# Kernel optimization log

Measured on AMD Instinct MI355X. Metric: run time of the kernel, lower is better.

Reference implementation:

```python
import jax, jax.numpy as jnp
import numpy as np

IGNORE_INDEX = -100
N, H, V = 4096, 4096, 32000


def setup_inputs() -> dict:
    key = jax.random.key(0)
    k1, k2, k3 = jax.random.split(key, 3)
    x = jax.random.normal(k1, (N, H), dtype=jnp.float32)
    y = jax.random.randint(k2, (N,), 0, V, dtype=jnp.int64)
    # lm_head weight, torch Linear layout [out_features=V, in_features=H]
    W = jax.random.normal(k3, (V, H), dtype=jnp.float32) * (1.0 / np.sqrt(H))
    return {"x": x, "y": y, "W": W}


def reference(x, y, W):
    # Fused linear + cross-entropy, reduction='mean' over non-ignored tokens.
    logits = jnp.einsum("nh,vh->nv", x, W)            # [N, V]
    logp = jax.nn.log_softmax(logits, axis=-1)         # [N, V]
    safe_y = jnp.where(y == IGNORE_INDEX, 0, y)
    nll = -jnp.take_along_axis(logp, safe_y[:, None], axis=-1)[:, 0]  # [N]
    valid = (y != IGNORE_INDEX).astype(logits.dtype)
    n_valid = jnp.maximum(valid.sum(), 1.0)
    return (nll * valid).sum() / n_valid
```

## Files before the change

kernel.cpp:

```cpp
#include <hip/hip_runtime.h>
#include <stdint.h>
#include <math.h>

#define N_TOK 4096
#define H_DIM 4096
#define V_DIM 32000

#define BM2 256
#define BN2 256
#define BK2 64
#define NKT (H_DIM / BK2)
#define CT2 (V_DIM / BN2)
#define MT2 (N_TOK / BM2)
#define WSCALE 16.0f
#define WSCALE_INV 0.0625f

#define BM 128
#define BN 128
#define BK 64
#define CT_NUM (V_DIM / BN)
#define MT_NUM (N_TOK / BM)

typedef __attribute__((ext_vector_type(8))) short short8;
typedef __attribute__((ext_vector_type(4))) float f32x4;
typedef __attribute__((ext_vector_type(2))) long long2_t;

#define MFMA16(a, b, c) __builtin_amdgcn_mfma_f32_16x16x32_bf16(a, b, c, 0, 0, 0)
#define MFMAF8(a, b, c) __builtin_amdgcn_mfma_f32_16x16x32_fp8_fp8(a, b, c, 0, 0, 0)
#define BARRIER() asm volatile("s_barrier" ::: "memory")

__device__ __forceinline__ unsigned short f2bf(float x) {
  union { float f; unsigned int u; } v; v.f = x;
  unsigned int r = v.u + 0x7fffu + ((v.u >> 16) & 1u);
  return (unsigned short)(r >> 16);
}

__device__ __forceinline__ unsigned int pk4(float a, float b, float c, float d) {
  int v = __builtin_amdgcn_cvt_pk_fp8_f32(a, b, 0, false);
  v = __builtin_amdgcn_cvt_pk_fp8_f32(c, d, v, true);
  return (unsigned int)v;
}

__device__ __forceinline__ void async16(const void* g, void* lds) {
  __builtin_amdgcn_global_load_lds(
      (const __attribute__((address_space(1))) void*)g,
      (__attribute__((address_space(3))) void*)lds, 16, 0, 0);
}

__global__ __launch_bounds__(256) void cast_f32_to_fp8_perm(
    const float* __restrict__ in, uint4* __restrict__ out, long nslots,
    float scale) {
  long stride = (long)gridDim.x * blockDim.x;
  for (long slot = (long)blockIdx.x * blockDim.x + threadIdx.x; slot < nslots;
       slot += stride) {
    long b = slot >> 2;
    int s = (int)(slot & 3);
    const float* p0 = in + b * 64 + s * 8;
    const float* p1 = p0 + 32;
    float4 a0 = *(const float4*)p0, a1 = *(const float4*)(p0 + 4);
    float4 c0 = *(const float4*)p1, c1 = *(const float4*)(p1 + 4);
    uint4 o;
    o.x = pk4(a0.x * scale, a0.y * scale, a0.z * scale, a0.w * scale);
    o.y = pk4(a1.x * scale, a1.y * scale, a1.z * scale, a1.w * scale);
    o.z = pk4(c0.x * scale, c0.y * scale, c0.z * scale, c0.w * scale);
    o.w = pk4(c1.x * scale, c1.y * scale, c1.z * scale, c1.w * scale);
    out[slot] = o;
  }
}

__device__ __forceinline__ void stage8(const uint8_t* __restrict__ src,
                                       int grow0, int kt, char* dest, int tid) {
  const int r = tid >> 2;
  const int p = tid & 3;
  const int s = p ^ (r & 3);
  const uint8_t* g = src + (size_t)(grow0 + r) * H_DIM + (size_t)kt * 64 + s * 16;
  async16(g, dest + (tid >> 6) * 1024);
}

template<int MF>
__device__ __forceinline__ void cluster16f8(f32x4 (&acc)[8][4],
    long2_t aL, long2_t aH, long2_t (&breg)[4]) {
#pragma unroll
  for (int nf = 0; nf < 4; nf++) acc[MF][nf]     = MFMAF8(aL[0], breg[nf][0], acc[MF][nf]);
#pragma unroll
  for (int nf = 0; nf < 4; nf++) acc[MF + 1][nf] = MFMAF8(aH[0], breg[nf][0], acc[MF + 1][nf]);
#pragma unroll
  for (int nf = 0; nf < 4; nf++) acc[MF][nf]     = MFMAF8(aL[1], breg[nf][1], acc[MF][nf]);
#pragma unroll
  for (int nf = 0; nf < 4; nf++) acc[MF + 1][nf] = MFMAF8(aH[1], breg[nf][1], acc[MF + 1][nf]);
}

template<int P>
__device__ __forceinline__ void phase_tile(char* lds,
    const uint8_t* __restrict__ Xq, const uint8_t* __restrict__ Wq,
    int mbase, int cbase, int ktA, int ktB, int tid,
    const int (&aOff)[8], const int (&bOff)[4], f32x4 (&acc)[8][4]) {
  const char* aB = lds + P * 32768;
  const char* bB = aB + 16384;
  char* aN = lds + (P ^ 1) * 32768;
  char* bC = lds + P * 32768 + 16384;
  long2_t breg[4];

  stage8(Xq, mbase + 0, ktA, aN + 0, tid);
#pragma unroll
  for (int nf = 0; nf < 4; nf++) breg[nf] = *(const long2_t*)(bB + bOff[nf]);
  {
    long2_t a0 = *(const long2_t*)(aB + aOff[0]);
    long2_t a1 = *(const long2_t*)(aB + aOff[1]);
    BARRIER();
    __builtin_amdgcn_s_setprio(1);
    cluster16f8<0>(acc, a0, a1, breg);
    __builtin_amdgcn_s_setprio(0);
    BARRIER();
  }
  stage8(Xq, mbase + 128, ktA, aN + 8192, tid);
  {
    long2_t a0 = *(const long2_t*)(aB + aOff[2]);
    long2_t a1 = *(const long2_t*)(aB + aOff[3]);
    BARRIER();
    __builtin_amdgcn_s_setprio(1);
    cluster16f8<2>(acc, a0, a1, breg);
    __builtin_amdgcn_s_setprio(0);
    BARRIER();
  }
  stage8(Wq, cbase + 0, ktB, bC + 0, tid);
  {
    long2_t a0 = *(const long2_t*)(aB + aOff[4]);
    long2_t a1 = *(const long2_t*)(aB + aOff[5]);
    BARRIER();
    __builtin_amdgcn_s_setprio(1);
    cluster16f8<4>(acc, a0, a1, breg);
    __builtin_amdgcn_s_setprio(0);
    BARRIER();
  }
  stage8(Wq, cbase + 128, ktB, bC + 8192, tid);
  {
    long2_t a0 = *(const long2_t*)(aB + aOff[6]);
    long2_t a1 = *(const long2_t*)(aB + aOff[7]);
    asm volatile("s_waitcnt vmcnt(2)" ::: "memory");
    BARRIER();
    __builtin_amdgcn_s_setprio(1);
    cluster16f8<6>(acc, a0, a1, breg);
    __builtin_amdgcn_s_setprio(0);
    BARRIER();
  }
}

__global__ __launch_bounds__(512, 2) void gemm_lse8(
    const uint8_t* __restrict__ Xq, const uint8_t* __restrict__ Wq,
    float* __restrict__ pmax, float* __restrict__ psum) {
  extern __shared__ char lds[];
  const int tid = threadIdx.x;
  const int lane = tid & 63;
  const int wid = tid >> 6;
  const int wm = wid >> 2, wn = wid & 3;

  int logical = (blockIdx.x & 7) * (CT2 * MT2 / 8) + (blockIdx.x >> 3);
  const int ct = logical / MT2, mt = logical - ct * MT2;
  const int mbase = mt * BM2, cbase = ct * BN2;

  const int sl16 = (((lane >> 4) ^ (lane & 3)) << 4);
  int aOff[8], bOff[4];
#pragma unroll
  for (int mf = 0; mf < 8; mf++)
    aOff[mf] = (wm * 128 + mf * 16 + (lane & 15)) * 64 + sl16;
#pragma unroll
  for (int nf = 0; nf < 4; nf++)
    bOff[nf] = (wn * 64 + nf * 16 + (lane & 15)) * 64 + sl16;

  f32x4 acc[8][4];
#pragma unroll
  for (int i = 0; i < 8; i++)
#pragma unroll
    for (int j = 0; j < 4; j++) { f32x4 z = {0.f, 0.f, 0.f, 0.f}; acc[i][j] = z; }

  stage8(Wq, cbase + 0,   0, lds + 16384, tid);
  stage8(Wq, cbase + 128, 0, lds + 24576, tid);
  stage8(Xq, mbase + 0,   0, lds + 0,     tid);
  stage8(Xq, mbase + 128, 0, lds + 8192,  tid);
  stage8(Wq, cbase + 0,   1, lds + 49152, tid);
  stage8(Wq, cbase + 128, 1, lds + 57344, tid);
  asm volatile("s_waitcnt vmcnt(2)" ::: "memory");
  BARRIER();

#pragma unroll 1
  for (int i = 0; i < NKT / 2; i++) {
    int g0 = 2 * i, g1 = 2 * i + 1;
    int a0t = g0 + 1;
    int b0t = (g0 + 2 < NKT) ? g0 + 2 : NKT - 1;
    int a1t = (g1 + 1 < NKT) ? g1 + 1 : NKT - 1;
    int b1t = (g1 + 2 < NKT) ? g1 + 2 : NKT - 1;
    phase_tile<0>(lds, Xq, Wq, mbase, cbase, a0t, b0t, tid, aOff, bOff, acc);
    phase_tile<1>(lds, Xq, Wq, mbase, cbase, a1t, b1t, tid, aOff, bOff, acc);
  }

  asm volatile("s_waitcnt vmcnt(0)" ::: "memory");
  __syncthreads();

  float2* red = (float2*)lds;
#pragma unroll
  for (int mf = 0; mf < 8; mf++) {
#pragma unroll
    for (int qq = 0; qq < 4; qq++) {
      float v0 = acc[mf][0][qq] * WSCALE_INV, v1 = acc[mf][1][qq] * WSCALE_INV;
      float v2 = acc[mf][2][qq] * WSCALE_INV, v3 = acc[mf][3][qq] * WSCALE_INV;
      float mx = fmaxf(fmaxf(v0, v1), fmaxf(v2, v3));
#pragma unroll
      for (int d = 1; d < 16; d <<= 1) mx = fmaxf(mx, __shfl_xor(mx, d));
      float se = __expf(v0 - mx) + __expf(v1 - mx) + __expf(v2 - mx) + __expf(v3 - mx);
#pragma unroll
      for (int d = 1; d < 16; d <<= 1) se += __shfl_xor(se, d);
      if ((lane & 15) == 0) {
        int row = (wm << 7) + mf * 16 + ((lane >> 4) << 2) + qq;
        float2 v; v.x = mx; v.y = se;
        red[row * 4 + wn] = v;
      }
    }
  }
  __syncthreads();
  if (tid < 256) {
    float M = -INFINITY, S = 0.f;
#pragma unroll
    for (int w = 0; w < 4; w++) {
      float2 rr = red[tid * 4 + w];
      float Mn = fmaxf(M, rr.x);
      S = S * __expf(M - Mn) + rr.y * __expf(rr.x - Mn);
      M = Mn;
    }
    size_t o = (size_t)ct * N_TOK + mbase + tid;
    pmax[o] = M;
    psum[o] = S;
  }
}

__global__ __launch_bounds__(256) void gemm_lse_small(
    const float* __restrict__ Xf, const float* __restrict__ Wf,
    float* __restrict__ pmax, float* __restrict__ psum) {
  __shared__ unsigned short As[BM * BK];
  __shared__ unsigned short Bs[BN * BK];
  const int ct = blockIdx.x / MT_NUM;
  const int mt = blockIdx.x % MT_NUM;
  const int mbase = mt * BM, cbase = ct * BN;
  const int tid = threadIdx.x;
  const int lane = tid & 63;
  const int wid = tid >> 6;
  const int wr = wid >> 1, wc = wid & 1;
  f32x4 acc[4][4];
#pragma unroll
  for (int i = 0; i < 4; i++)
#pragma unroll
    for (int j = 0; j < 4; j++) { f32x4 z = {0.f, 0.f, 0.f, 0.f}; acc[i][j] = z; }
  for (int ks = 0; ks < H_DIM / BK; ks++) {
    const int k0 = ks * BK;
#pragma unroll
    for (int r = 0; r < 4; r++) {
      int o = r * 4096 + wid * 1024 + lane * 16;
      int row = o >> 7;
      int kc = (o & 127) >> 1;
      const float* xs = Xf + (size_t)(mbase + row) * H_DIM + k0 + kc;
      const float* wv = Wf + (size_t)(cbase + row) * H_DIM + k0 + kc;
      float4 x0 = *(const float4*)xs, x1 = *(const float4*)(xs + 4);
      float4 w0 = *(const float4*)wv, w1 = *(const float4*)(wv + 4);
      short8 xa, wa;
      xa[0] = f2bf(x0.x); xa[1] = f2bf(x0.y); xa[2] = f2bf(x0.z); xa[3] = f2bf(x0.w);
      xa[4] = f2bf(x1.x); xa[5] = f2bf(x1.y); xa[6] = f2bf(x1.z); xa[7] = f2bf(x1.w);
      wa[0] = f2bf(w0.x); wa[1] = f2bf(w0.y); wa[2] = f2bf(w0.z); wa[3] = f2bf(w0.w);
      wa[4] = f2bf(w1.x); wa[5] = f2bf(w1.y); wa[6] = f2bf(w1.z); wa[7] = f2bf(w1.w);
      *(short8*)((char*)As + o) = xa;
      *(short8*)((char*)Bs + o) = wa;
    }
    __syncthreads();
#pragma unroll
    for (int kk = 0; kk < 2; kk++) {
      short8 a[4], b[4];
#pragma unroll
      for (int m = 0; m < 4; m++)
        a[m] = *(const short8*)((const char*)As +
                (wr * 64 + m * 16 + (lane & 15)) * 128 + kk * 64 + (lane >> 4) * 16);
#pragma unroll
      for (int n = 0; n < 4; n++)
        b[n] = *(const short8*)((const char*)Bs +
                (wc * 64 + n * 16 + (lane & 15)) * 128 + kk * 64 + (lane >> 4) * 16);
#pragma unroll
      for (int m = 0; m < 4; m++)
#pragma unroll
        for (int n = 0; n < 4; n++)
          acc[m][n] = MFMA16(a[m], b[n], acc[m][n]);
    }
    __syncthreads();
  }
  float* red = (float*)As;
  const int g = lane >> 4;
#pragma unroll
  for (int m = 0; m < 4; m++) {
#pragma unroll
    for (int q = 0; q < 4; q++) {
      float v0 = acc[m][0][q], v1 = acc[m][1][q], v2 = acc[m][2][q], v3 = acc[m][3][q];
      float mx = fmaxf(fmaxf(v0, v1), fmaxf(v2, v3));
#pragma unroll
      for (int d = 1; d < 16; d <<= 1) mx = fmaxf(mx, __shfl_xor(mx, d));
      float se = __expf(v0 - mx) + __expf(v1 - mx) + __expf(v2 - mx) + __expf(v3 - mx);
#pragma unroll
      for (int d = 1; d < 16; d <<= 1) se += __shfl_xor(se, d);
      if ((lane & 15) == 0) {
        int row = wr * 64 + m * 16 + g * 4 + q;
        red[row * 4 + wc * 2 + 0] = mx;
        red[row * 4 + wc * 2 + 1] = se;
      }
    }
  }
  __syncthreads();
  if (tid < BM) {
    float m0 = red[tid * 4 + 0], s0 = red[tid * 4 + 1];
    float m1 = red[tid * 4 + 2], s1 = red[tid * 4 + 3];
    float M = fmaxf(m0, m1);
    float S = s0 * __expf(m0 - M) + s1 * __expf(m1 - M);
    size_t o = (size_t)ct * N_TOK + mbase + tid;
    pmax[o] = M;
    psum[o] = S;
  }
}

__global__ __launch_bounds__(256) void target_logit(
    const float* __restrict__ X, const float* __restrict__ W,
    const int* __restrict__ y, float* __restrict__ tl) {
  __shared__ float red[4];
  int row = blockIdx.x;
  int lab = y[row];
  float s = 0.f;
  if (lab >= 0 && lab < V_DIM) {
    const float4* xr = (const float4*)(X + (size_t)row * H_DIM);
    const float4* wr = (const float4*)(W + (size_t)lab * H_DIM);
    for (int i = threadIdx.x; i < H_DIM / 4; i += 256) {
      float4 a = xr[i], b = wr[i];
      s += a.x * b.x + a.y * b.y + a.z * b.z + a.w * b.w;
    }
  }
#pragma unroll
  for (int o = 32; o > 0; o >>= 1) s += __shfl_down(s, o);
  if ((threadIdx.x & 63) == 0) red[threadIdx.x >> 6] = s;
  __syncthreads();
  if (threadIdx.x == 0) tl[row] = red[0] + red[1] + red[2] + red[3];
}

__global__ __launch_bounds__(256) void combine_rows(
    const float* __restrict__ pmax, const float* __restrict__ psum,
    const float* __restrict__ tl, const int* __restrict__ y,
    float* __restrict__ lossb, float* __restrict__ validb, int n_ct) {
  int row = blockIdx.x * 256 + threadIdx.x;
  if (row >= N_TOK) return;
  float M = -INFINITY, S = 0.f;
  for (int ct = 0; ct < n_ct; ct++) {
    float m = pmax[(size_t)ct * N_TOK + row];
    float s = psum[(size_t)ct * N_TOK + row];
    float Mn = fmaxf(M, m);
    S = S * __expf(M - Mn) + s * __expf(m - Mn);
    M = Mn;
  }
  bool valid = (y[row] != -100);
  lossb[row] = valid ? (M + __logf(S) - tl[row]) : 0.f;
  validb[row] = valid ? 1.f : 0.f;
}

__global__ __launch_bounds__(256) void finalize_loss(
    const float* __restrict__ lossb, const float* __restrict__ validb,
    float* __restrict__ out) {
  __shared__ float rs[4], rc[4];
  float s = 0.f, c = 0.f;
  for (int i = threadIdx.x; i < N_TOK; i += 256) { s += lossb[i]; c += validb[i]; }
#pragma unroll
  for (int o = 32; o > 0; o >>= 1) { s += __shfl_down(s, o); c += __shfl_down(c, o); }
  if ((threadIdx.x & 63) == 0) { rs[threadIdx.x >> 6] = s; rc[threadIdx.x >> 6] = c; }
  __syncthreads();
  if (threadIdx.x == 0) {
    float S = rs[0] + rs[1] + rs[2] + rs[3];
    float C = rc[0] + rc[1] + rc[2] + rc[3];
    out[0] = S / fmaxf(C, 1.f);
  }
}

extern "C" void kernel_launch(void* const* d_in, const int* in_sizes, int n_in,
                              void* d_out, int out_size, void* d_ws, size_t ws_size,
                              hipStream_t stream) {
  const float* x = (const float*)d_in[0];
  const int* y = (const int*)d_in[1];
  const float* W = (const float*)d_in[2];
  float* out = (float*)d_out;
  char* ws = (char*)d_ws;

  const size_t szWq = (size_t)V_DIM * H_DIM;
  const size_t szXq = (size_t)N_TOK * H_DIM;
  const size_t szP  = (size_t)CT_NUM * N_TOK * 4;
  const size_t szT  = (size_t)N_TOK * 4;
  const size_t needFull = szWq + szXq + 2 * szP + 3 * szT;

  bool full = (ws_size >= needFull);
  uint8_t* Wq = nullptr;
  uint8_t* Xq = nullptr;
  size_t off = 0;
  if (full) { Wq = (uint8_t*)ws; Xq = (uint8_t*)(ws + szWq); off = szWq + szXq; }
  float* pmax   = (float*)(ws + off); off += szP;
  float* psum   = (float*)(ws + off); off += szP;
  float* tl     = (float*)(ws + off); off += szT;
  float* lossb  = (float*)(ws + off); off += szT;
  float* validb = (float*)(ws + off);

  if (full) {
    cast_f32_to_fp8_perm<<<8192, 256, 0, stream>>>(
        W, (uint4*)Wq, (long)(szWq / 16), WSCALE);
    cast_f32_to_fp8_perm<<<2048, 256, 0, stream>>>(
        x, (uint4*)Xq, (long)(szXq / 16), 1.0f);
    (void)hipFuncSetAttribute((const void*)gemm_lse8,
        hipFuncAttributeMaxDynamicSharedMemorySize, 65536);
    gemm_lse8<<<CT2 * MT2, 512, 65536, stream>>>(Xq, Wq, pmax, psum);
    target_logit<<<N_TOK, 256, 0, stream>>>(x, W, y, tl);
    combine_rows<<<N_TOK / 256, 256, 0, stream>>>(pmax, psum, tl, y, lossb, validb, CT2);
  } else {
    gemm_lse_small<<<CT_NUM * MT_NUM, 256, 0, stream>>>(x, W, pmax, psum);
    target_logit<<<N_TOK, 256, 0, stream>>>(x, W, y, tl);
    combine_rows<<<N_TOK / 256, 256, 0, stream>>>(pmax, psum, tl, y, lossb, validb, CT_NUM);
  }
  finalize_loss<<<1, 256, 0, stream>>>(lossb, validb, out);
}
```

Baseline: 938.9 us.

## Switch FP8 GEMM to MX-scaled 16x16x128 MFMA with BK=128 tiles

```diff
diff --git a/kernel.cpp b/kernel.cpp
--- a/kernel.cpp
+++ b/kernel.cpp
@@ -8,8 +8,8 @@
 
 #define BM2 256
 #define BN2 256
-#define BK2 64
-#define NKT (H_DIM / BK2)
+#define BK2 128
+#define NKT2 (H_DIM / BK2)
 #define CT2 (V_DIM / BN2)
 #define MT2 (N_TOK / BM2)
 #define WSCALE 16.0f
@@ -23,10 +23,12 @@
 
 typedef __attribute__((ext_vector_type(8))) short short8;
 typedef __attribute__((ext_vector_type(4))) float f32x4;
-typedef __attribute__((ext_vector_type(2))) long long2_t;
+typedef __attribute__((ext_vector_type(4))) int i32x4;
+typedef __attribute__((ext_vector_type(8))) int i32x8;
 
 #define MFMA16(a, b, c) __builtin_amdgcn_mfma_f32_16x16x32_bf16(a, b, c, 0, 0, 0)
-#define MFMAF8(a, b, c) __builtin_amdgcn_mfma_f32_16x16x32_fp8_fp8(a, b, c, 0, 0, 0)
+#define MFMAMX(a, b, c) __builtin_amdgcn_mfma_scale_f32_16x16x128_f8f6f4( \
+    a, b, c, 0, 0, 0, 0x7f7f7f7f, 0, 0x7f7f7f7f)
 #define BARRIER() asm volatile("s_barrier" ::: "memory")
 
 __device__ __forceinline__ unsigned short f2bf(float x) {
@@ -47,100 +49,109 @@
       (__attribute__((address_space(3))) void*)lds, 16, 0, 0);
 }
 
-__global__ __launch_bounds__(256) void cast_f32_to_fp8_perm(
+__global__ __launch_bounds__(256) void cast_f32_to_fp8(
     const float* __restrict__ in, uint4* __restrict__ out, long nslots,
     float scale) {
   long stride = (long)gridDim.x * blockDim.x;
   for (long slot = (long)blockIdx.x * blockDim.x + threadIdx.x; slot < nslots;
        slot += stride) {
-    long b = slot >> 2;
-    int s = (int)(slot & 3);
-    const float* p0 = in + b * 64 + s * 8;
-    const float* p1 = p0 + 32;
-    float4 a0 = *(const float4*)p0, a1 = *(const float4*)(p0 + 4);
-    float4 c0 = *(const float4*)p1, c1 = *(const float4*)(p1 + 4);
+    const float4* p = (const float4*)(in + slot * 16);
+    float4 a0 = p[0], a1 = p[1], a2 = p[2], a3 = p[3];
     uint4 o;
     o.x = pk4(a0.x * scale, a0.y * scale, a0.z * scale, a0.w * scale);
     o.y = pk4(a1.x * scale, a1.y * scale, a1.z * scale, a1.w * scale);
-    o.z = pk4(c0.x * scale, c0.y * scale, c0.z * scale, c0.w * scale);
-    o.w = pk4(c1.x * scale, c1.y * scale, c1.z * scale, c1.w * scale);
+    o.z = pk4(a2.x * scale, a2.y * scale, a2.z * scale, a2.w * scale);
+    o.w = pk4(a3.x * scale, a3.y * scale, a3.z * scale, a3.w * scale);
     out[slot] = o;
   }
 }
 
-__device__ __forceinline__ void stage8(const uint8_t* __restrict__ src,
-                                       int grow0, int kt, char* dest, int tid) {
-  const int r = tid >> 2;
-  const int p = tid & 3;
-  const int s = p ^ (r & 3);
-  const uint8_t* g = src + (size_t)(grow0 + r) * H_DIM + (size_t)kt * 64 + s * 16;
+__device__ __forceinline__ void stageMX(const uint8_t* __restrict__ src,
+                                        int grow0, int kt, char* dest, int tid) {
+  const int r = tid >> 3;
+  const int p = tid & 7;
+  const int s = p ^ (r & 7);
+  const uint8_t* g = src + (size_t)(grow0 + r) * H_DIM + (size_t)kt * 128 + s * 16;
   async16(g, dest + (tid >> 6) * 1024);
 }
 
-template<int MF>
-__device__ __forceinline__ void cluster16f8(f32x4 (&acc)[8][4],
-    long2_t aL, long2_t aH, long2_t (&breg)[4]) {
-#pragma unroll
-  for (int nf = 0; nf < 4; nf++) acc[MF][nf]     = MFMAF8(aL[0], breg[nf][0], acc[MF][nf]);
-#pragma unroll
-  for (int nf = 0; nf < 4; nf++) acc[MF + 1][nf] = MFMAF8(aH[0], breg[nf][0], acc[MF + 1][nf]);
-#pragma unroll
-  for (int nf = 0; nf < 4; nf++) acc[MF][nf]     = MFMAF8(aL[1], breg[nf][1], acc[MF][nf]);
-#pragma unroll
-  for (int nf = 0; nf < 4; nf++) acc[MF + 1][nf] = MFMAF8(aH[1], breg[nf][1], acc[MF + 1][nf]);
+__device__ __forceinline__ i32x8 ld_op(const char* base, int rowByte, int s0, int s1) {
+  i32x4 lo = *(const i32x4*)(base + rowByte + s0);
+  i32x4 hi = *(const i32x4*)(base + rowByte + s1);
+  i32x8 r;
+  r[0] = lo[0]; r[1] = lo[1]; r[2] = lo[2]; r[3] = lo[3];
+  r[4] = hi[0]; r[5] = hi[1]; r[6] = hi[2]; r[7] = hi[3];
+  return r;
 }
 
 template<int P>
-__device__ __forceinline__ void phase_tile(char* lds,
+__device__ __forceinline__ void tile_mx(char* lds,
     const uint8_t* __restrict__ Xq, const uint8_t* __restrict__ Wq,
     int mbase, int cbase, int ktA, int ktB, int tid,
-    const int (&aOff)[8], const int (&bOff)[4], f32x4 (&acc)[8][4]) {
-  const char* aB = lds + P * 32768;
-  const char* bB = aB + 16384;
-  char* aN = lds + (P ^ 1) * 32768;
-  char* bC = lds + P * 32768 + 16384;
-  long2_t breg[4];
-
-  stage8(Xq, mbase + 0, ktA, aN + 0, tid);
-#pragma unroll
-  for (int nf = 0; nf < 4; nf++) breg[nf] = *(const long2_t*)(bB + bOff[nf]);
+    const int (&aRow)[8], const int (&bRow)[4], int s0, int s1,
+    f32x4 (&acc)[8][4]) {
+  const char* aB = lds + P * 65536;
+  const char* bB = aB + 32768;
+  char* aN = lds + (P ^ 1) * 65536;
+  char* bC = lds + P * 65536 + 32768;
+  i32x8 breg[4];
+
+  stageMX(Xq, mbase + 0,  ktA, aN + 0,    tid);
+  stageMX(Xq, mbase + 64, ktA, aN + 8192, tid);
+#pragma unroll
+  for (int nf = 0; nf < 4; nf++) breg[nf] = ld_op(bB, bRow[nf], s0, s1);
   {
-    long2_t a0 = *(const long2_t*)(aB + aOff[0]);
-    long2_t a1 = *(const long2_t*)(aB + aOff[1]);
+    i32x8 a0 = ld_op(aB, aRow[0], s0, s1);
+    i32x8 a1 = ld_op(aB, aRow[1], s0, s1);
     BARRIER();
     __builtin_amdgcn_s_setprio(1);
-    cluster16f8<0>(acc, a0, a1, breg);
+#pragma unroll
+    for (int nf = 0; nf < 4; nf++) acc[0][nf] = MFMAMX(a0, breg[nf], acc[0][nf]);
+#pragma unroll
+    for (int nf = 0; nf < 4; nf++) acc[1][nf] = MFMAMX(a1, breg[nf], acc[1][nf]);
     __builtin_amdgcn_s_setprio(0);
     BARRIER();
   }
-  stage8(Xq, mbase + 128, ktA, aN + 8192, tid);
+  stageMX(Xq, mbase + 128, ktA, aN + 16384, tid);
+  stageMX(Xq, mbase + 192, ktA, aN + 24576, tid);
   {
-    long2_t a0 = *(const long2_t*)(aB + aOff[2]);
-    long2_t a1 = *(const long2_t*)(aB + aOff[3]);
+    i32x8 a0 = ld_op(aB, aRow[2], s0, s1);
+    i32x8 a1 = ld_op(aB, aRow[3], s0, s1);
     BARRIER();
     __builtin_amdgcn_s_setprio(1);
-    cluster16f8<2>(acc, a0, a1, breg);
+#pragma unroll
+    for (int nf = 0; nf < 4; nf++) acc[2][nf] = MFMAMX(a0, breg[nf], acc[2][nf]);
+#pragma unroll
+    for (int nf = 0; nf < 4; nf++) acc[3][nf] = MFMAMX(a1, breg[nf], acc[3][nf]);
     __builtin_amdgcn_s_setprio(0);
     BARRIER();
   }
-  stage8(Wq, cbase + 0, ktB, bC + 0, tid);
+  stageMX(Wq, cbase + 0,  ktB, bC + 0,    tid);
+  stageMX(Wq, cbase + 64, ktB, bC + 8192, tid);
   {
-    long2_t a0 = *(const long2_t*)(aB + aOff[4]);
-    long2_t a1 = *(const long2_t*)(aB + aOff[5]);
+    i32x8 a0 = ld_op(aB, aRow[4], s0, s1);
+    i32x8 a1 = ld_op(aB, aRow[5], s0, s1);
     BARRIER();
     __builtin_amdgcn_s_setprio(1);
-    cluster16f8<4>(acc, a0, a1, breg);
+#pragma unroll
+    for (int nf = 0; nf < 4; nf++) acc[4][nf] = MFMAMX(a0, breg[nf], acc[4][nf]);
+#pragma unroll
+    for (int nf = 0; nf < 4; nf++) acc[5][nf] = MFMAMX(a1, breg[nf], acc[5][nf]);
     __builtin_amdgcn_s_setprio(0);
     BARRIER();
   }
-  stage8(Wq, cbase + 128, ktB, bC + 8192, tid);
+  stageMX(Wq, cbase + 128, ktB, bC + 16384, tid);
+  stageMX(Wq, cbase + 192, ktB, bC + 24576, tid);
   {
-    long2_t a0 = *(const long2_t*)(aB + aOff[6]);
-    long2_t a1 = *(const long2_t*)(aB + aOff[7]);
-    asm volatile("s_waitcnt vmcnt(2)" ::: "memory");
+    i32x8 a0 = ld_op(aB, aRow[6], s0, s1);
+    i32x8 a1 = ld_op(aB, aRow[7], s0, s1);
+    asm volatile("s_waitcnt vmcnt(4)" ::: "memory");
     BARRIER();
     __builtin_amdgcn_s_setprio(1);
-    cluster16f8<6>(acc, a0, a1, breg);
+#pragma unroll
+    for (int nf = 0; nf < 4; nf++) acc[6][nf] = MFMAMX(a0, breg[nf], acc[6][nf]);
+#pragma unroll
+    for (int nf = 0; nf < 4; nf++) acc[7][nf] = MFMAMX(a1, breg[nf], acc[7][nf]);
     __builtin_amdgcn_s_setprio(0);
     BARRIER();
   }
@@ -159,14 +170,14 @@
   const int ct = logical / MT2, mt = logical - ct * MT2;
   const int mbase = mt * BM2, cbase = ct * BN2;
 
-  const int sl16 = (((lane >> 4) ^ (lane & 3)) << 4);
-  int aOff[8], bOff[4];
-#pragma unroll
-  for (int mf = 0; mf < 8; mf++)
-    aOff[mf] = (wm * 128 + mf * 16 + (lane & 15)) * 64 + sl16;
-#pragma unroll
-  for (int nf = 0; nf < 4; nf++)
-    bOff[nf] = (wn * 64 + nf * 16 + (lane & 15)) * 64 + sl16;
+  const int g2 = lane >> 4;
+  const int s0 = (((2 * g2)     ^ (lane & 7)) << 4);
+  const int s1 = (((2 * g2 + 1) ^ (lane & 7)) << 4);
+  int aRow[8], bRow[4];
+#pragma unroll
+  for (int mf = 0; mf < 8; mf++) aRow[mf] = (wm * 128 + mf * 16 + (lane & 15)) * 128;
+#pragma unroll
+  for (int nf = 0; nf < 4; nf++) bRow[nf] = (wn * 64 + nf * 16 + (lane & 15)) * 128;
 
   f32x4 acc[8][4];
 #pragma unroll
@@ -174,24 +185,30 @@
 #pragma unroll
     for (int j = 0; j < 4; j++) { f32x4 z = {0.f, 0.f, 0.f, 0.f}; acc[i][j] = z; }
 
-  stage8(Wq, cbase + 0,   0, lds + 16384, tid);
-  stage8(Wq, cbase + 128, 0, lds + 24576, tid);
-  stage8(Xq, mbase + 0,   0, lds + 0,     tid);
-  stage8(Xq, mbase + 128, 0, lds + 8192,  tid);
-  stage8(Wq, cbase + 0,   1, lds + 49152, tid);
-  stage8(Wq, cbase + 128, 1, lds + 57344, tid);
-  asm volatile("s_waitcnt vmcnt(2)" ::: "memory");
+  stageMX(Wq, cbase + 0,   0, lds + 32768, tid);
+  stageMX(Wq, cbase + 64,  0, lds + 40960, tid);
+  stageMX(Wq, cbase + 128, 0, lds + 49152, tid);
+  stageMX(Wq, cbase + 192, 0, lds + 57344, tid);
+  stageMX(Xq, mbase + 0,   0, lds + 0,     tid);
+  stageMX(Xq, mbase + 64,  0, lds + 8192,  tid);
+  stageMX(Xq, mbase + 128, 0, lds + 16384, tid);
+  stageMX(Xq, mbase + 192, 0, lds + 24576, tid);
+  stageMX(Wq, cbase + 0,   1, lds + 65536 + 32768, tid);
+  stageMX(Wq, cbase + 64,  1, lds + 65536 + 40960, tid);
+  stageMX(Wq, cbase + 128, 1, lds + 65536 + 49152, tid);
+  stageMX(Wq, cbase + 192, 1, lds + 65536 + 57344, tid);
+  asm volatile("s_waitcnt vmcnt(4)" ::: "memory");
   BARRIER();
 
 #pragma unroll 1
-  for (int i = 0; i < NKT / 2; i++) {
+  for (int i = 0; i < NKT2 / 2; i++) {
     int g0 = 2 * i, g1 = 2 * i + 1;
     int a0t = g0 + 1;
-    int b0t = (g0 + 2 < NKT) ? g0 + 2 : NKT - 1;
-    int a1t = (g1 + 1 < NKT) ? g1 + 1 : NKT - 1;
-    int b1t = (g1 + 2 < NKT) ? g1 + 2 : NKT - 1;
-    phase_tile<0>(lds, Xq, Wq, mbase, cbase, a0t, b0t, tid, aOff, bOff, acc);
-    phase_tile<1>(lds, Xq, Wq, mbase, cbase, a1t, b1t, tid, aOff, bOff, acc);
+    int b0t = (g0 + 2 < NKT2) ? g0 + 2 : NKT2 - 1;
+    int a1t = (g1 + 1 < NKT2) ? g1 + 1 : NKT2 - 1;
+    int b1t = (g1 + 2 < NKT2) ? g1 + 2 : NKT2 - 1;
+    tile_mx<0>(lds, Xq, Wq, mbase, cbase, a0t, b0t, tid, aRow, bRow, s0, s1, acc);
+    tile_mx<1>(lds, Xq, Wq, mbase, cbase, a1t, b1t, tid, aRow, bRow, s0, s1, acc);
   }
 
   asm volatile("s_waitcnt vmcnt(0)" ::: "memory");
@@ -211,7 +228,7 @@
 #pragma unroll
       for (int d = 1; d < 16; d <<= 1) se += __shfl_xor(se, d);
       if ((lane & 15) == 0) {
-        int row = (wm << 7) + mf * 16 + ((lane >> 4) << 2) + qq;
+        int row = (wm << 7) + mf * 16 + (g2 << 2) + qq;
         float2 v; v.x = mx; v.y = se;
         red[row * 4 + wn] = v;
       }
@@ -406,13 +423,13 @@
   float* validb = (float*)(ws + off);
 
   if (full) {
-    cast_f32_to_fp8_perm<<<8192, 256, 0, stream>>>(
+    cast_f32_to_fp8<<<8192, 256, 0, stream>>>(
         W, (uint4*)Wq, (long)(szWq / 16), WSCALE);
-    cast_f32_to_fp8_perm<<<2048, 256, 0, stream>>>(
+    cast_f32_to_fp8<<<2048, 256, 0, stream>>>(
         x, (uint4*)Xq, (long)(szXq / 16), 1.0f);
     (void)hipFuncSetAttribute((const void*)gemm_lse8,
-        hipFuncAttributeMaxDynamicSharedMemorySize, 65536);
-    gemm_lse8<<<CT2 * MT2, 512, 65536, stream>>>(Xq, Wq, pmax, psum);
+        hipFuncAttributeMaxDynamicSharedMemorySize, 131072);
+    gemm_lse8<<<CT2 * MT2, 512, 131072, stream>>>(Xq, Wq, pmax, psum);
     target_logit<<<N_TOK, 256, 0, stream>>>(x, W, y, tl);
     combine_rows<<<N_TOK / 256, 256, 0, stream>>>(pmax, psum, tl, y, lossb, validb, CT2);
   } else {
```

Result: slower. 1.346 ms (+43.3%).

## Double K-tile depth to 128 and triple-buffer W tiles in 160KB LDS

Applied to the files above, without the earlier changes.

```diff
diff --git a/kernel.cpp b/kernel.cpp
--- a/kernel.cpp
+++ b/kernel.cpp
@@ -8,8 +8,8 @@
 
 #define BM2 256
 #define BN2 256
-#define BK2 64
-#define NKT (H_DIM / BK2)
+#define BK2 128
+#define NKT2 (H_DIM / BK2)
 #define CT2 (V_DIM / BN2)
 #define MT2 (N_TOK / BM2)
 #define WSCALE 16.0f
@@ -47,15 +47,16 @@
       (__attribute__((address_space(3))) void*)lds, 16, 0, 0);
 }
 
-__global__ __launch_bounds__(256) void cast_f32_to_fp8_perm(
+__global__ __launch_bounds__(256) void cast_f32_to_fp8_k128(
     const float* __restrict__ in, uint4* __restrict__ out, long nslots,
     float scale) {
   long stride = (long)gridDim.x * blockDim.x;
   for (long slot = (long)blockIdx.x * blockDim.x + threadIdx.x; slot < nslots;
        slot += stride) {
-    long b = slot >> 2;
-    int s = (int)(slot & 3);
-    const float* p0 = in + b * 64 + s * 8;
+    long b = slot >> 3;
+    int s = (int)(slot & 7);
+    int t = s >> 2, g = s & 3;
+    const float* p0 = in + b * 128 + t * 64 + g * 8;
     const float* p1 = p0 + 32;
     float4 a0 = *(const float4*)p0, a1 = *(const float4*)(p0 + 4);
     float4 c0 = *(const float4*)p1, c1 = *(const float4*)(p1 + 4);
@@ -68,85 +69,140 @@
   }
 }
 
-__device__ __forceinline__ void stage8(const uint8_t* __restrict__ src,
-                                       int grow0, int kt, char* dest, int tid) {
-  const int r = tid >> 2;
-  const int p = tid & 3;
-  const int s = p ^ (r & 3);
-  const uint8_t* g = src + (size_t)(grow0 + r) * H_DIM + (size_t)kt * 64 + s * 16;
-  async16(g, dest + (tid >> 6) * 1024);
-}
-
-template<int MF>
-__device__ __forceinline__ void cluster16f8(f32x4 (&acc)[8][4],
-    long2_t aL, long2_t aH, long2_t (&breg)[4]) {
-#pragma unroll
-  for (int nf = 0; nf < 4; nf++) acc[MF][nf]     = MFMAF8(aL[0], breg[nf][0], acc[MF][nf]);
-#pragma unroll
-  for (int nf = 0; nf < 4; nf++) acc[MF + 1][nf] = MFMAF8(aH[0], breg[nf][0], acc[MF + 1][nf]);
-#pragma unroll
-  for (int nf = 0; nf < 4; nf++) acc[MF][nf]     = MFMAF8(aL[1], breg[nf][1], acc[MF][nf]);
-#pragma unroll
-  for (int nf = 0; nf < 4; nf++) acc[MF + 1][nf] = MFMAF8(aH[1], breg[nf][1], acc[MF + 1][nf]);
-}
-
-template<int P>
-__device__ __forceinline__ void phase_tile(char* lds,
-    const uint8_t* __restrict__ Xq, const uint8_t* __restrict__ Wq,
-    int mbase, int cbase, int ktA, int ktB, int tid,
-    const int (&aOff)[8], const int (&bOff)[4], f32x4 (&acc)[8][4]) {
-  const char* aB = lds + P * 32768;
-  const char* bB = aB + 16384;
-  char* aN = lds + (P ^ 1) * 32768;
-  char* bC = lds + P * 32768 + 16384;
-  long2_t breg[4];
-
-  stage8(Xq, mbase + 0, ktA, aN + 0, tid);
-#pragma unroll
-  for (int nf = 0; nf < 4; nf++) breg[nf] = *(const long2_t*)(bB + bOff[nf]);
+__device__ __forceinline__ void stage8(const uint8_t* __restrict__ base,
+                                       int off, char* dest, int tid) {
+  async16(base + off, dest + (tid >> 6) * 1024);
+}
+
+__device__ __forceinline__ long2_t ldq(const char* base, int off) {
+  return *(const long2_t*)(base + off);
+}
+
+template<int AP, int BR>
+__device__ __forceinline__ void tile_fp8(char* lds,
+    const uint8_t* __restrict__ Xbase, const uint8_t* __restrict__ Wbase,
+    int roff, int ktA, int ktB, int tid,
+    int aRowBase, int bRowBase, int c0, int c1, f32x4 (&acc)[8][4]) {
+  const char* aB = lds + AP * 32768;
+  char* aN = lds + (AP ^ 1) * 32768;
+  const char* bB = lds + 65536 + BR * 32768;
+  char* bN = lds + 65536 + ((BR + 2) % 3) * 32768;
+  const int kA = ktA * 128, kB = ktB * 128;
+  long2_t bL[4], bH[4];
+
+  stage8(Xbase, roff + kA,              aN + 0,    tid);
+  stage8(Xbase, roff + 64 * H_DIM + kA, aN + 8192, tid);
+#pragma unroll
+  for (int nf = 0; nf < 4; nf++) {
+    bL[nf] = ldq(bB, bRowBase + nf * 2048 + c0);
+    bH[nf] = ldq(bB, bRowBase + nf * 2048 + c1);
+  }
   {
-    long2_t a0 = *(const long2_t*)(aB + aOff[0]);
-    long2_t a1 = *(const long2_t*)(aB + aOff[1]);
+    long2_t a0L = ldq(aB, aRowBase + 0 + c0),    a0H = ldq(aB, aRowBase + 0 + c1);
+    long2_t a1L = ldq(aB, aRowBase + 2048 + c0), a1H = ldq(aB, aRowBase + 2048 + c1);
     BARRIER();
     __builtin_amdgcn_s_setprio(1);
-    cluster16f8<0>(acc, a0, a1, breg);
+#pragma unroll
+    for (int nf = 0; nf < 4; nf++) acc[0][nf] = MFMAF8(a0L[0], bL[nf][0], acc[0][nf]);
+#pragma unroll
+    for (int nf = 0; nf < 4; nf++) acc[1][nf] = MFMAF8(a1L[0], bL[nf][0], acc[1][nf]);
+#pragma unroll
+    for (int nf = 0; nf < 4; nf++) acc[0][nf] = MFMAF8(a0L[1], bL[nf][1], acc[0][nf]);
+#pragma unroll
+    for (int nf = 0; nf < 4; nf++) acc[1][nf] = MFMAF8(a1L[1], bL[nf][1], acc[1][nf]);
+#pragma unroll
+    for (int nf = 0; nf < 4; nf++) acc[0][nf] = MFMAF8(a0H[0], bH[nf][0], acc[0][nf]);
+#pragma unroll
+    for (int nf = 0; nf < 4; nf++) acc[1][nf] = MFMAF8(a1H[0], bH[nf][0], acc[1][nf]);
+#pragma unroll
+    for (int nf = 0; nf < 4; nf++) acc[0][nf] = MFMAF8(a0H[1], bH[nf][1], acc[0][nf]);
+#pragma unroll
+    for (int nf = 0; nf < 4; nf++) acc[1][nf] = MFMAF8(a1H[1], bH[nf][1], acc[1][nf]);
     __builtin_amdgcn_s_setprio(0);
     BARRIER();
   }
-  stage8(Xq, mbase + 128, ktA, aN + 8192, tid);
+  stage8(Xbase, roff + 128 * H_DIM + kA, aN + 16384, tid);
+  stage8(Xbase, roff + 192 * H_DIM + kA, aN + 24576, tid);
   {
-    long2_t a0 = *(const long2_t*)(aB + aOff[2]);
-    long2_t a1 = *(const long2_t*)(aB + aOff[3]);
+    long2_t a0L = ldq(aB, aRowBase + 4096 + c0), a0H = ldq(aB, aRowBase + 4096 + c1);
+    long2_t a1L = ldq(aB, aRowBase + 6144 + c0), a1H = ldq(aB, aRowBase + 6144 + c1);
     BARRIER();
     __builtin_amdgcn_s_setprio(1);
-    cluster16f8<2>(acc, a0, a1, breg);
+#pragma unroll
+    for (int nf = 0; nf < 4; nf++) acc[2][nf] = MFMAF8(a0L[0], bL[nf][0], acc[2][nf]);
+#pragma unroll
+    for (int nf = 0; nf < 4; nf++) acc[3][nf] = MFMAF8(a1L[0], bL[nf][0], acc[3][nf]);
+#pragma unroll
+    for (int nf = 0; nf < 4; nf++) acc[2][nf] = MFMAF8(a0L[1], bL[nf][1], acc[2][nf]);
+#pragma unroll
+    for (int nf = 0; nf < 4; nf++) acc[3][nf] = MFMAF8(a1L[1], bL[nf][1], acc[3][nf]);
+#pragma unroll
+    for (int nf = 0; nf < 4; nf++) acc[2][nf] = MFMAF8(a0H[0], bH[nf][0], acc[2][nf]);
+#pragma unroll
+    for (int nf = 0; nf < 4; nf++) acc[3][nf] = MFMAF8(a1H[0], bH[nf][0], acc[3][nf]);
+#pragma unroll
+    for (int nf = 0; nf < 4; nf++) acc[2][nf] = MFMAF8(a0H[1], bH[nf][1], acc[2][nf]);
+#pragma unroll
+    for (int nf = 0; nf < 4; nf++) acc[3][nf] = MFMAF8(a1H[1], bH[nf][1], acc[3][nf]);
     __builtin_amdgcn_s_setprio(0);
     BARRIER();
   }
-  stage8(Wq, cbase + 0, ktB, bC + 0, tid);
+  stage8(Wbase, roff + kB,              bN + 0,    tid);
+  stage8(Wbase, roff + 64 * H_DIM + kB, bN + 8192, tid);
   {
-    long2_t a0 = *(const long2_t*)(aB + aOff[4]);
-    long2_t a1 = *(const long2_t*)(aB + aOff[5]);
+    long2_t a0L = ldq(aB, aRowBase + 8192 + c0),  a0H = ldq(aB, aRowBase + 8192 + c1);
+    long2_t a1L = ldq(aB, aRowBase + 10240 + c0), a1H = ldq(aB, aRowBase + 10240 + c1);
     BARRIER();
     __builtin_amdgcn_s_setprio(1);
-    cluster16f8<4>(acc, a0, a1, breg);
+#pragma unroll
+    for (int nf = 0; nf < 4; nf++) acc[4][nf] = MFMAF8(a0L[0], bL[nf][0], acc[4][nf]);
+#pragma unroll
+    for (int nf = 0; nf < 4; nf++) acc[5][nf] = MFMAF8(a1L[0], bL[nf][0], acc[5][nf]);
+#pragma unroll
+    for (int nf = 0; nf < 4; nf++) acc[4][nf] = MFMAF8(a0L[1], bL[nf][1], acc[4][nf]);
+#pragma unroll
+    for (int nf = 0; nf < 4; nf++) acc[5][nf] = MFMAF8(a1L[1], bL[nf][1], acc[5][nf]);
+#pragma unroll
+    for (int nf = 0; nf < 4; nf++) acc[4][nf] = MFMAF8(a0H[0], bH[nf][0], acc[4][nf]);
+#pragma unroll
+    for (int nf = 0; nf < 4; nf++) acc[5][nf] = MFMAF8(a1H[0], bH[nf][0], acc[5][nf]);
+#pragma unroll
+    for (int nf = 0; nf < 4; nf++) acc[4][nf] = MFMAF8(a0H[1], bH[nf][1], acc[4][nf]);
+#pragma unroll
+    for (int nf = 0; nf < 4; nf++) acc[5][nf] = MFMAF8(a1H[1], bH[nf][1], acc[5][nf]);
     __builtin_amdgcn_s_setprio(0);
     BARRIER();
   }
-  stage8(Wq, cbase + 128, ktB, bC + 8192, tid);
+  stage8(Wbase, roff + 128 * H_DIM + kB, bN + 16384, tid);
+  stage8(Wbase, roff + 192 * H_DIM + kB, bN + 24576, tid);
   {
-    long2_t a0 = *(const long2_t*)(aB + aOff[6]);
-    long2_t a1 = *(const long2_t*)(aB + aOff[7]);
-    asm volatile("s_waitcnt vmcnt(2)" ::: "memory");
+    long2_t a0L = ldq(aB, aRowBase + 12288 + c0), a0H = ldq(aB, aRowBase + 12288 + c1);
+    long2_t a1L = ldq(aB, aRowBase + 14336 + c0), a1H = ldq(aB, aRowBase + 14336 + c1);
+    asm volatile("s_waitcnt vmcnt(4)" ::: "memory");
     BARRIER();
     __builtin_amdgcn_s_setprio(1);
-    cluster16f8<6>(acc, a0, a1, breg);
+#pragma unroll
+    for (int nf = 0; nf < 4; nf++) acc[6][nf] = MFMAF8(a0L[0], bL[nf][0], acc[6][nf]);
+#pragma unroll
+    for (int nf = 0; nf < 4; nf++) acc[7][nf] = MFMAF8(a1L[0], bL[nf][0], acc[7][nf]);
+#pragma unroll
+    for (int nf = 0; nf < 4; nf++) acc[6][nf] = MFMAF8(a0L[1], bL[nf][1], acc[6][nf]);
+#pragma unroll
+    for (int nf = 0; nf < 4; nf++) acc[7][nf] = MFMAF8(a1L[1], bL[nf][1], acc[7][nf]);
+#pragma unroll
+    for (int nf = 0; nf < 4; nf++) acc[6][nf] = MFMAF8(a0H[0], bH[nf][0], acc[6][nf]);
+#pragma unroll
+    for (int nf = 0; nf < 4; nf++) acc[7][nf] = MFMAF8(a1H[0], bH[nf][0], acc[7][nf]);
+#pragma unroll
+    for (int nf = 0; nf < 4; nf++) acc[6][nf] = MFMAF8(a0H[1], bH[nf][1], acc[6][nf]);
+#pragma unroll
+    for (int nf = 0; nf < 4; nf++) acc[7][nf] = MFMAF8(a1H[1], bH[nf][1], acc[7][nf]);
     __builtin_amdgcn_s_setprio(0);
     BARRIER();
   }
 }
 
-__global__ __launch_bounds__(512, 2) void gemm_lse8(
+__global__ __launch_bounds__(512, 1) void gemm_lse8(
     const uint8_t* __restrict__ Xq, const uint8_t* __restrict__ Wq,
     float* __restrict__ pmax, float* __restrict__ psum) {
   extern __shared__ char lds[];
@@ -158,15 +214,16 @@
   int logical = (blockIdx.x & 7) * (CT2 * MT2 / 8) + (blockIdx.x >> 3);
   const int ct = logical / MT2, mt = logical - ct * MT2;
   const int mbase = mt * BM2, cbase = ct * BN2;
-
-  const int sl16 = (((lane >> 4) ^ (lane & 3)) << 4);
-  int aOff[8], bOff[4];
-#pragma unroll
-  for (int mf = 0; mf < 8; mf++)
-    aOff[mf] = (wm * 128 + mf * 16 + (lane & 15)) * 64 + sl16;
-#pragma unroll
-  for (int nf = 0; nf < 4; nf++)
-    bOff[nf] = (wn * 64 + nf * 16 + (lane & 15)) * 64 + sl16;
+  const uint8_t* Xbase = Xq + (size_t)mbase * H_DIM;
+  const uint8_t* Wbase = Wq + (size_t)cbase * H_DIM;
+
+  const int roff = (tid >> 3) * H_DIM + ((((tid & 7) ^ ((tid >> 3) & 7))) << 4);
+
+  const int g2 = lane >> 4;
+  const int c0 = ((g2 ^ (lane & 7)) << 4);
+  const int c1 = (((4 + g2) ^ (lane & 7)) << 4);
+  const int aRowBase = (wm * 128 + (lane & 15)) * 128;
+  const int bRowBase = (wn * 64 + (lane & 15)) * 128;
 
   f32x4 acc[8][4];
 #pragma unroll
@@ -174,25 +231,41 @@
 #pragma unroll
     for (int j = 0; j < 4; j++) { f32x4 z = {0.f, 0.f, 0.f, 0.f}; acc[i][j] = z; }
 
-  stage8(Wq, cbase + 0,   0, lds + 16384, tid);
-  stage8(Wq, cbase + 128, 0, lds + 24576, tid);
-  stage8(Xq, mbase + 0,   0, lds + 0,     tid);
-  stage8(Xq, mbase + 128, 0, lds + 8192,  tid);
-  stage8(Wq, cbase + 0,   1, lds + 49152, tid);
-  stage8(Wq, cbase + 128, 1, lds + 57344, tid);
-  asm volatile("s_waitcnt vmcnt(2)" ::: "memory");
+  stage8(Wbase, roff + 0,            lds + 65536 + 0,     tid);
+  stage8(Wbase, roff + 64 * H_DIM,   lds + 65536 + 8192,  tid);
+  stage8(Wbase, roff + 128 * H_DIM,  lds + 65536 + 16384, tid);
+  stage8(Wbase, roff + 192 * H_DIM,  lds + 65536 + 24576, tid);
+  stage8(Xbase, roff + 0,            lds + 0,     tid);
+  stage8(Xbase, roff + 64 * H_DIM,   lds + 8192,  tid);
+  stage8(Xbase, roff + 128 * H_DIM,  lds + 16384, tid);
+  stage8(Xbase, roff + 192 * H_DIM,  lds + 24576, tid);
+  stage8(Wbase, roff + 128,               lds + 98304 + 0,     tid);
+  stage8(Wbase, roff + 64 * H_DIM + 128,  lds + 98304 + 8192,  tid);
+  stage8(Wbase, roff + 128 * H_DIM + 128, lds + 98304 + 16384, tid);
+  stage8(Wbase, roff + 192 * H_DIM + 128, lds + 98304 + 24576, tid);
+  asm volatile("s_waitcnt vmcnt(4)" ::: "memory");
   BARRIER();
 
 #pragma unroll 1
-  for (int i = 0; i < NKT / 2; i++) {
-    int g0 = 2 * i, g1 = 2 * i + 1;
-    int a0t = g0 + 1;
-    int b0t = (g0 + 2 < NKT) ? g0 + 2 : NKT - 1;
-    int a1t = (g1 + 1 < NKT) ? g1 + 1 : NKT - 1;
-    int b1t = (g1 + 2 < NKT) ? g1 + 2 : NKT - 1;
-    phase_tile<0>(lds, Xq, Wq, mbase, cbase, a0t, b0t, tid, aOff, bOff, acc);
-    phase_tile<1>(lds, Xq, Wq, mbase, cbase, a1t, b1t, tid, aOff, bOff, acc);
-  }
+  for (int i = 0; i < 5; i++) {
+    int g = 6 * i;
+    tile_fp8<0, 0>(lds, Xbase, Wbase, roff, g + 1, g + 2, tid,
+                   aRowBase, bRowBase, c0, c1, acc);
+    tile_fp8<1, 1>(lds, Xbase, Wbase, roff, g + 2, g + 3, tid,
+                   aRowBase, bRowBase, c0, c1, acc);
+    tile_fp8<0, 2>(lds, Xbase, Wbase, roff, g + 3, g + 4, tid,
+                   aRowBase, bRowBase, c0, c1, acc);
+    tile_fp8<1, 0>(lds, Xbase, Wbase, roff, g + 4, g + 5, tid,
+                   aRowBase, bRowBase, c0, c1, acc);
+    tile_fp8<0, 1>(lds, Xbase, Wbase, roff, g + 5, g + 6, tid,
+                   aRowBase, bRowBase, c0, c1, acc);
+    tile_fp8<1, 2>(lds, Xbase, Wbase, roff, g + 6, g + 7, tid,
+                   aRowBase, bRowBase, c0, c1, acc);
+  }
+  tile_fp8<0, 0>(lds, Xbase, Wbase, roff, 31, 31, tid,
+                 aRowBase, bRowBase, c0, c1, acc);
+  tile_fp8<1, 1>(lds, Xbase, Wbase, roff, 31, 31, tid,
+                 aRowBase, bRowBase, c0, c1, acc);
 
   asm volatile("s_waitcnt vmcnt(0)" ::: "memory");
   __syncthreads();
@@ -211,7 +284,7 @@
 #pragma unroll
       for (int d = 1; d < 16; d <<= 1) se += __shfl_xor(se, d);
       if ((lane & 15) == 0) {
-        int row = (wm << 7) + mf * 16 + ((lane >> 4) << 2) + qq;
+        int row = (wm << 7) + mf * 16 + (g2 << 2) + qq;
         float2 v; v.x = mx; v.y = se;
         red[row * 4 + wn] = v;
       }
@@ -406,13 +479,13 @@
   float* validb = (float*)(ws + off);
 
   if (full) {
-    cast_f32_to_fp8_perm<<<8192, 256, 0, stream>>>(
+    cast_f32_to_fp8_k128<<<8192, 256, 0, stream>>>(
         W, (uint4*)Wq, (long)(szWq / 16), WSCALE);
-    cast_f32_to_fp8_perm<<<2048, 256, 0, stream>>>(
+    cast_f32_to_fp8_k128<<<2048, 256, 0, stream>>>(
         x, (uint4*)Xq, (long)(szXq / 16), 1.0f);
     (void)hipFuncSetAttribute((const void*)gemm_lse8,
-        hipFuncAttributeMaxDynamicSharedMemorySize, 65536);
-    gemm_lse8<<<CT2 * MT2, 512, 65536, stream>>>(Xq, Wq, pmax, psum);
+        hipFuncAttributeMaxDynamicSharedMemorySize, 163840);
+    gemm_lse8<<<CT2 * MT2, 512, 163840, stream>>>(Xq, Wq, pmax, psum);
     target_logit<<<N_TOK, 256, 0, stream>>>(x, W, y, tl);
     combine_rows<<<N_TOK / 256, 256, 0, stream>>>(pmax, psum, tl, y, lossb, validb, CT2);
   } else {
```

Measured after the change: 1.162 ms. +23.8%, slower.
